# Performance work log

Measured on AMD Instinct MI355X. Metric: run time of the kernel, lower is better.

The kernel has to match this reference:

```python
import jax, jax.numpy as jnp
import numpy as np

# ---- config (mirrors cfg / init kwargs) ----
FEAT_STRIDE = 16
IM_DIMS = (1024, 1024)          # (height, width)
ANCHOR_SCALES = (8, 16, 32)
ANCHOR_RATIOS = (0.5, 1.0, 2.0)
PRE_NMS_TOPN = 6000             # eval mode (cfg_key=1)
POST_NMS_TOPN = 300
NMS_THRESH = 0.7
MIN_SIZE = 16


def _generate_base_anchors(base_size=16, ratios=ANCHOR_RATIOS, scales=ANCHOR_SCALES):
    """py-faster-rcnn generate_anchors, in numpy (static)."""
    def mk(ws, hs, xc, yc):
        return np.stack([xc - 0.5 * (ws - 1), yc - 0.5 * (hs - 1),
                         xc + 0.5 * (ws - 1), yc + 0.5 * (hs - 1)], axis=1)
    base = np.array([0, 0, base_size - 1, base_size - 1], dtype=np.float64)
    w = base[2] - base[0] + 1; h = base[3] - base[1] + 1
    xc = base[0] + 0.5 * (w - 1); yc = base[1] + 0.5 * (h - 1)
    # ratio enum
    size = w * h
    ws = np.round(np.sqrt(size / np.array(ratios)))
    hs = np.round(ws * np.array(ratios))
    ratio_anchors = mk(ws, hs, xc, yc)
    # scale enum
    out = []
    for a in ratio_anchors:
        aw = a[2] - a[0] + 1; ah = a[3] - a[1] + 1
        axc = a[0] + 0.5 * (aw - 1); ayc = a[1] + 0.5 * (ah - 1)
        out.append(mk(aw * np.array(scales), ah * np.array(scales), axc, ayc))
    return np.concatenate(out, axis=0).astype(np.float32)  # [A,4]


def _all_anchors(H, W):
    base = _generate_base_anchors()                       # [A,4]
    sx = np.arange(W) * FEAT_STRIDE
    sy = np.arange(H) * FEAT_STRIDE
    sx, sy = np.meshgrid(sx, sy)
    shifts = np.stack([sx.ravel(), sy.ravel(), sx.ravel(), sy.ravel()], axis=1)  # [H*W,4]
    anchors = shifts[:, None, :].astype(np.float32) + base[None, :, :]
    return anchors.reshape(-1, 4)                         # [H*W*A, 4]


def setup_inputs() -> dict:
    key = jax.random.key(0)
    k1, k2 = jax.random.split(key)
    H, W, A = 64, 64, 9
    rpn_cls_score = jax.random.normal(k1, (1, H, W, 2 * A), dtype=jnp.float32)
    rpn_bbox_pred = jax.random.normal(k2, (1, H, W, 4 * A), dtype=jnp.float32)
    return {"rpn_cls_score": rpn_cls_score, "rpn_bbox_pred": rpn_bbox_pred}


def _proposals(rpn_cls_score, rpn_bbox_pred):
    _, H, W, C2 = rpn_cls_score.shape
    A = C2 // 2
    # rpn_softmax: per-anchor 2-way softmax, foreground prob
    scores = jax.nn.softmax(rpn_cls_score.reshape(H, W, A, 2), axis=-1)[..., 1].reshape(-1)  # [N]
    deltas = rpn_bbox_pred.reshape(-1, 4)                  # [N,4]
    anchors = jnp.asarray(_all_anchors(H, W))              # [N,4]
    # bbox_transform_inv
    aw = anchors[:, 2] - anchors[:, 0] + 1.0
    ah = anchors[:, 3] - anchors[:, 1] + 1.0
    axc = anchors[:, 0] + 0.5 * aw
    ayc = anchors[:, 1] + 0.5 * ah
    dx, dy, dw, dh = deltas[:, 0], deltas[:, 1], deltas[:, 2], deltas[:, 3]
    pxc = dx * aw + axc; pyc = dy * ah + ayc
    pw = jnp.exp(dw) * aw; ph = jnp.exp(dh) * ah
    x1 = pxc - 0.5 * pw; y1 = pyc - 0.5 * ph
    x2 = pxc + 0.5 * pw; y2 = pyc + 0.5 * ph
    # clip to image
    im_h, im_w = IM_DIMS
    x1 = jnp.clip(x1, 0.0, im_w - 1.0); x2 = jnp.clip(x2, 0.0, im_w - 1.0)
    y1 = jnp.clip(y1, 0.0, im_h - 1.0); y2 = jnp.clip(y2, 0.0, im_h - 1.0)
    boxes = jnp.stack([x1, y1, x2, y2], axis=1)            # [N,4]
    # filter too-small boxes by masking their score
    valid = ((x2 - x1 + 1.0) >= MIN_SIZE) & ((y2 - y1 + 1.0) >= MIN_SIZE)
    scores = jnp.where(valid, scores, -jnp.inf)
    return boxes, scores


def _nms_keep(boxes, K):
    """Greedy NMS keep-mask over score-descending boxes [K,4]."""
    x1, y1, x2, y2 = boxes[:, 0], boxes[:, 1], boxes[:, 2], boxes[:, 3]
    areas = (x2 - x1 + 1.0) * (y2 - y1 + 1.0)
    ix1 = jnp.maximum(x1[:, None], x1[None, :])
    iy1 = jnp.maximum(y1[:, None], y1[None, :])
    ix2 = jnp.minimum(x2[:, None], x2[None, :])
    iy2 = jnp.minimum(y2[:, None], y2[None, :])
    iw = jnp.maximum(ix2 - ix1 + 1.0, 0.0)
    ih = jnp.maximum(iy2 - iy1 + 1.0, 0.0)
    inter = iw * ih
    iou = inter / (areas[:, None] + areas[None, :] - inter)  # [K,K]
    idxs = jnp.arange(K)
    def body(i, keep):
        sup = keep[i] & (iou[i] > NMS_THRESH) & (idxs > i)
        return keep & ~sup
    return jax.lax.fori_loop(0, K, body, jnp.ones((K,), bool))


def reference(rpn_cls_score, rpn_bbox_pred):
    boxes, scores = _proposals(rpn_cls_score, rpn_bbox_pred)
    K = min(PRE_NMS_TOPN, scores.shape[0])
    top_scores, order = jax.lax.top_k(scores, K)           # score-descending
    top_boxes = boxes[order]                               # [K,4]
    keep = _nms_keep(top_boxes, K)
    sel_scores = jnp.where(keep, top_scores, -jnp.inf)
    _, idx = jax.lax.top_k(sel_scores, POST_NMS_TOPN)      # kept, in score order
    out_boxes = top_boxes[idx]                             # [post,4]
    blob = jnp.concatenate([jnp.zeros((POST_NMS_TOPN, 1), out_boxes.dtype), out_boxes], axis=1)
    return blob                                            # [post,5] (batch_idx, x1,y1,x2,y2)
```

## Files before the change

kernel.cpp:

```cpp
#include <hip/hip_runtime.h>
#include <stdint.h>

typedef unsigned long long u64;
typedef unsigned int u32;

#define N_ANCH 36864
#define WGRID 64
#define A_PER 9
#define KTOP 6000
#define NOUT 300
#define NBIN 8192
#define NCHK 94
#define INF_BIN 0

__constant__ float c_ax1[9] = {-84.f,-176.f,-360.f,-56.f,-120.f,-248.f,-36.f,-80.f,-168.f};
__constant__ float c_ay1[9] = {-40.f,-88.f,-184.f,-56.f,-120.f,-248.f,-80.f,-168.f,-344.f};
__constant__ float c_aw[9]  = {184.f,368.f,736.f,128.f,256.f,512.f,88.f,176.f,352.f};
__constant__ float c_ah[9]  = {96.f,192.f,384.f,128.f,256.f,512.f,176.f,352.f,704.f};

__device__ __forceinline__ u32 binof(u32 u) {
    if (u < 0x80000000u) return 0u;
    if (u < 0xBF000000u) return 1u + ((u - 0x80000000u) >> 22);
    return 256u + ((u - 0xBF000000u) >> 11);
}

__global__ __launch_bounds__(1024) void proposal_kernel(const float* __restrict__ cls,
                                                        const float* __restrict__ dlt,
                                                        u64* __restrict__ keys,
                                                        float4* __restrict__ boxes,
                                                        u32* __restrict__ hist) {
    __shared__ u32 lh[NBIN];
    const int t = threadIdx.x;
    for (int b = t; b < NBIN; b += 1024) lh[b] = 0;
    __syncthreads();

    int i = blockIdx.x * 1024 + t;
    int a  = i % A_PER;
    int hw = i / A_PER;
    int wx = hw % WGRID;
    int hy = hw / WGRID;

    float l0 = cls[hw * 18 + 2 * a];
    float l1 = cls[hw * 18 + 2 * a + 1];
    float m  = fmaxf(l0, l1);
    float e0 = expf(l0 - m), e1 = expf(l1 - m);
    float s  = e1 / (e0 + e1);

    const float* d = dlt + hw * 36 + 4 * a;
    float dx = d[0], dy = d[1], dw = d[2], dh = d[3];
    float aw = c_aw[a], ah = c_ah[a];
    float axc = (c_ax1[a] + 16.f * (float)wx) + 0.5f * aw;
    float ayc = (c_ay1[a] + 16.f * (float)hy) + 0.5f * ah;

    float pxc = dx * aw + axc;
    float pyc = dy * ah + ayc;
    float pw  = expf(dw) * aw;
    float ph  = expf(dh) * ah;
    float x1 = pxc - 0.5f * pw, y1 = pyc - 0.5f * ph;
    float x2 = pxc + 0.5f * pw, y2 = pyc + 0.5f * ph;
    x1 = fminf(fmaxf(x1, 0.f), 1023.f);
    x2 = fminf(fmaxf(x2, 0.f), 1023.f);
    y1 = fminf(fmaxf(y1, 0.f), 1023.f);
    y2 = fminf(fmaxf(y2, 0.f), 1023.f);
    bool valid = ((x2 - x1 + 1.f) >= 16.f) && ((y2 - y1 + 1.f) >= 16.f);
    float sc = valid ? s : -__builtin_huge_valf();

    u32 sb  = __float_as_uint(sc);
    u32 ord = (sb & 0x80000000u) ? ~sb : (sb | 0x80000000u);
    u64 key = ((u64)ord << 32) | (u32)(~(u32)i);
    keys[i]  = key;
    boxes[i] = make_float4(x1, y1, x2, y2);

    u64 infb = __ballot(!valid);
    if (valid) {
        atomicAdd(&lh[binof(ord)], 1u);
    } else {
        int lane = t & 63;
        if (lane == __builtin_ctzll(infb))
            atomicAdd(&lh[INF_BIN], (u32)__popcll(infb));
    }
    __syncthreads();
    for (int b = t; b < NBIN; b += 1024) {
        u32 v = lh[b];
        if (v) atomicAdd(&hist[b], v);
    }
}

__global__ __launch_bounds__(1024) void scan_kernel(const u32* __restrict__ hist,
                                                    u32* __restrict__ binStart,
                                                    u32* __restrict__ gEV) {
    __shared__ u32 sh[1024];
    int t = threadIdx.x;
    if (t == 0) gEV[1] = KTOP;
    int hi = NBIN - 1 - 8 * t;
    u32 cnt[8];
    u32 sum = 0;
#pragma unroll
    for (int k = 0; k < 8; ++k) { cnt[k] = hist[hi - k]; sum += cnt[k]; }
    sh[t] = sum;
    __syncthreads();
    for (int d = 1; d < 1024; d <<= 1) {
        u32 v = (t >= d) ? sh[t - d] : 0;
        __syncthreads();
        sh[t] += v;
        __syncthreads();
    }
    u32 run = sh[t] - sum;
#pragma unroll
    for (int k = 0; k < 8; ++k) {
        int b = hi - k;
        binStart[b] = run;
        u32 end = run + cnt[k];
        if (run < KTOP && end >= KTOP) gEV[0] = end;
        run = end;
    }
}

__global__ void scatter_kernel(const u64* __restrict__ keys,
                               const u32* __restrict__ binStart,
                               u32* __restrict__ cursor,
                               u64* __restrict__ scat) {
    int i = blockIdx.x * blockDim.x + threadIdx.x;
    if (i >= N_ANCH) return;
    u64 k = keys[i];
    u32 b = binof((u32)(k >> 32));
    u32 s = binStart[b];
    if (s < KTOP) {
        u32 p = s + atomicAdd(&cursor[b], 1u);
        scat[p] = k;
    }
}

__global__ void rank_kernel(const u64* __restrict__ scat,
                            const u32* __restrict__ binStart,
                            const u32* __restrict__ hist,
                            const float4* __restrict__ boxes,
                            const u32* __restrict__ gEV,
                            float4* __restrict__ topBoxes,
                            int* __restrict__ gV) {
    int i = blockIdx.x * blockDim.x + threadIdx.x;
    u32 E = gEV[0];
    if (i >= (int)E) return;
    u64 k = scat[i];
    u32 b = binof((u32)(k >> 32));
    u32 s = binStart[b], c = hist[b];
    u32 r = s;
    for (u32 j = s; j < s + c; ++j) r += (scat[j] > k) ? 1u : 0u;
    if (r < KTOP) {
        int idx = (int)(~(u32)k);
        topBoxes[r] = boxes[idx];
        if (!(k >> 63)) atomicMin(gV, (int)r);
    }
}

__device__ __forceinline__ bool iou_gt(float4 a, float areaA, float4 b, float areaB) {
    float ix1 = fmaxf(a.x, b.x), iy1 = fmaxf(a.y, b.y);
    float ix2 = fminf(a.z, b.z), iy2 = fminf(a.w, b.w);
    float iw = fmaxf(ix2 - ix1 + 1.0f, 0.0f);
    float ih = fmaxf(iy2 - iy1 + 1.0f, 0.0f);
    float inter = iw * ih;
    float iou = inter / (areaA + areaB - inter);
    return iou > 0.7f;
}

__global__ __launch_bounds__(1024) void nms_out_kernel(const float4* __restrict__ topBoxes,
                                                       const u32* __restrict__ gEV,
                                                       float* __restrict__ out) {
    __shared__ float4 cbox[2][64];
    __shared__ float  ca[2][64];
    __shared__ u64    intra[2][64];
    __shared__ u64    supw[16];
    __shared__ u64    keepw[NCHK];
    __shared__ float4 kbox[NOUT];
    __shared__ float  karea[NOUT];
    __shared__ u32    scanbuf[1024];
    __shared__ int    s_nkept;

    const int t = threadIdx.x;
    const int lane = t & 63;
    const int w = t >> 6;
    if (t < NCHK) keepw[t] = 0;
    if (t == 0) s_nkept = 0;
    const int V = (int)gEV[1];
    const int nchunks = (V + 63) >> 6;

    if (t < 64) {
        float4 b = make_float4(0.f, 0.f, 0.f, 0.f);
        if (t < V) b = topBoxes[t];
        cbox[0][t] = b;
        ca[0][t]   = (b.z - b.x + 1.f) * (b.w - b.y + 1.f);
        intra[0][t] = 0;
    }
    __syncthreads();

    for (int c = 0; c < nchunks; ++c) {
        const int p = c & 1;
        const int base = c * 64;
        const int csz = min(64, V - base);
        const int nk = s_nkept;
        bool sup = false;
        if (lane < csz) {
            float4 bb = cbox[p][lane]; float ab = ca[p][lane];
            for (int k = w; k < nk; k += 16) {
                if (iou_gt(bb, ab, kbox[k], karea[k])) { sup = true; break; }
            }
        }
        u64 bal = __ballot(sup);
        if (lane == 0) supw[w] = bal;
        if (lane < csz) {
            float4 bb = cbox[p][lane]; float ab = ca[p][lane];
            u64 m = 0;
            int j0 = lane + 1;
            j0 += ((w - j0) % 16 + 16) % 16;
            for (int j = j0; j < csz; j += 16)
                if (iou_gt(bb, ab, cbox[p][j], ca[p][j])) m |= (1ULL << j);
            if (m) atomicOr(&intra[p][lane], m);
        }
        __syncthreads();
        if (w == 0) {
            u64 row = intra[p][lane];
            u64 sup64 = 0;
#pragma unroll
            for (int q = 0; q < 16; ++q) sup64 |= supw[q];
            u64 alive = ~sup64;
            if (csz < 64) alive &= ((1ULL << csz) - 1ULL);
            u64 cand = alive, kb = 0;
            const int nk_base = s_nkept;
            int nk2 = nk_base;
            while (cand && nk2 < NOUT) {
                int b = __builtin_ctzll(cand);
                cand &= cand - 1;
                kb |= (1ULL << b);
                ++nk2;
                cand &= ~__shfl(row, b, 64);
            }
            if ((kb >> lane) & 1ULL) {
                int pos = nk_base + __popcll(kb & ((1ULL << lane) - 1ULL));
                kbox[pos]  = cbox[p][lane];
                karea[pos] = ca[p][lane];
            }
            if (lane == 0) { keepw[c] = kb; s_nkept = nk2; }
        } else if (w == 1) {
            int nb = base + 64 + lane;
            float4 b = make_float4(0.f, 0.f, 0.f, 0.f);
            if (nb < V) b = topBoxes[nb];
            cbox[p ^ 1][lane] = b;
            ca[p ^ 1][lane]   = (b.z - b.x + 1.f) * (b.w - b.y + 1.f);
            intra[p ^ 1][lane] = 0;
        }
        __syncthreads();
        if (s_nkept >= NOUT) break;
    }

    const int n1 = s_nkept;
    for (int r = t; r < n1; r += 1024) {
        float4 b = kbox[r];
        out[r * 5 + 0] = 0.f;
        out[r * 5 + 1] = b.x; out[r * 5 + 2] = b.y;
        out[r * 5 + 3] = b.z; out[r * 5 + 4] = b.w;
    }
    if (n1 < NOUT) {
        __syncthreads();
        const int per = 6;
        int r0 = t * per, r1 = min(r0 + per, KTOP);
        u32 cnt = 0;
        for (int r = r0; r < r1; ++r)
            cnt += ((keepw[r >> 6] >> (r & 63)) & 1ULL) ? 0u : 1u;
        scanbuf[t] = cnt;
        __syncthreads();
        for (int d = 1; d < 1024; d <<= 1) {
            u32 v = (t >= d) ? scanbuf[t - d] : 0;
            __syncthreads();
            scanbuf[t] += v;
            __syncthreads();
        }
        int ord = n1 + (int)(scanbuf[t] - cnt);
        for (int r = r0; r < r1 && ord < NOUT; ++r) {
            if (!((keepw[r >> 6] >> (r & 63)) & 1ULL)) {
                float4 b = topBoxes[r];
                out[ord * 5 + 0] = 0.f;
                out[ord * 5 + 1] = b.x; out[ord * 5 + 2] = b.y;
                out[ord * 5 + 3] = b.z; out[ord * 5 + 4] = b.w;
                ++ord;
            }
        }
    }
}

extern "C" void kernel_launch(void* const* d_in, const int* in_sizes, int n_in,
                              void* d_out, int out_size, void* d_ws, size_t ws_size,
                              hipStream_t stream) {
    const float* cls = (const float*)d_in[0];
    const float* dlt = (const float*)d_in[1];
    float* out = (float*)d_out;
    char* ws = (char*)d_ws;
    u64*    keys     = (u64*)   (ws);
    u64*    scat     = (u64*)   (ws + 294912);
    float4* boxes    = (float4*)(ws + 589824);
    float4* topBoxes = (float4*)(ws + 1179648);
    u32*    hist     = (u32*)   (ws + 1275648);
    u32*    cursor   = (u32*)   (ws + 1308416);
    u32*    binStart = (u32*)   (ws + 1341184);
    u32*    gEV      = (u32*)   (ws + 1373952);

    hipMemsetAsync(hist, 0, 2 * NBIN * sizeof(u32), stream);
    proposal_kernel<<<36, 1024, 0, stream>>>(cls, dlt, keys, boxes, hist);
    scan_kernel<<<1, 1024, 0, stream>>>(hist, binStart, gEV);
    scatter_kernel<<<(N_ANCH + 255) / 256, 256, 0, stream>>>(keys, binStart, cursor, scat);
    rank_kernel<<<(N_ANCH + 255) / 256, 256, 0, stream>>>(scat, binStart, hist, boxes, gEV,
                                                          topBoxes, (int*)&gEV[1]);
    nms_out_kernel<<<1, 1024, 0, stream>>>(topBoxes, gEV, out);
}
```

Before: 118.2 us.

## Fuse proposal pipeline into one cooperative kernel and add spatial-grid NMS prefilter

Replaces the memset plus five separate launches with a single cooperative kernel of 36 blocks that uses grid.sync between the histogram, scan, scatter, rank and NMS phases. Keys stay in registers instead of round-tripping through global memory. It also adds a 64-bit coarse spatial occupancy signature per box, so IoU is only evaluated for pairs whose 128-pixel grid cells overlap. The costs are grid-wide barrier latency and cooperative-launch overhead, and the NMS tail still runs on only one block.

```diff
diff --git a/kernel.cpp b/kernel.cpp
--- a/kernel.cpp
+++ b/kernel.cpp
@@ -1,10 +1,14 @@
 #include <hip/hip_runtime.h>
+#include <hip/hip_cooperative_groups.h>
 #include <stdint.h>
+
+namespace cg = cooperative_groups;
 
 typedef unsigned long long u64;
 typedef unsigned int u32;
 
 #define N_ANCH 36864
+#define NBLK 36
 #define WGRID 64
 #define A_PER 9
 #define KTOP 6000
@@ -24,133 +28,12 @@
     return 256u + ((u - 0xBF000000u) >> 11);
 }
 
-__global__ __launch_bounds__(1024) void proposal_kernel(const float* __restrict__ cls,
-                                                        const float* __restrict__ dlt,
-                                                        u64* __restrict__ keys,
-                                                        float4* __restrict__ boxes,
-                                                        u32* __restrict__ hist) {
-    __shared__ u32 lh[NBIN];
-    const int t = threadIdx.x;
-    for (int b = t; b < NBIN; b += 1024) lh[b] = 0;
-    __syncthreads();
-
-    int i = blockIdx.x * 1024 + t;
-    int a  = i % A_PER;
-    int hw = i / A_PER;
-    int wx = hw % WGRID;
-    int hy = hw / WGRID;
-
-    float l0 = cls[hw * 18 + 2 * a];
-    float l1 = cls[hw * 18 + 2 * a + 1];
-    float m  = fmaxf(l0, l1);
-    float e0 = expf(l0 - m), e1 = expf(l1 - m);
-    float s  = e1 / (e0 + e1);
-
-    const float* d = dlt + hw * 36 + 4 * a;
-    float dx = d[0], dy = d[1], dw = d[2], dh = d[3];
-    float aw = c_aw[a], ah = c_ah[a];
-    float axc = (c_ax1[a] + 16.f * (float)wx) + 0.5f * aw;
-    float ayc = (c_ay1[a] + 16.f * (float)hy) + 0.5f * ah;
-
-    float pxc = dx * aw + axc;
-    float pyc = dy * ah + ayc;
-    float pw  = expf(dw) * aw;
-    float ph  = expf(dh) * ah;
-    float x1 = pxc - 0.5f * pw, y1 = pyc - 0.5f * ph;
-    float x2 = pxc + 0.5f * pw, y2 = pyc + 0.5f * ph;
-    x1 = fminf(fmaxf(x1, 0.f), 1023.f);
-    x2 = fminf(fmaxf(x2, 0.f), 1023.f);
-    y1 = fminf(fmaxf(y1, 0.f), 1023.f);
-    y2 = fminf(fmaxf(y2, 0.f), 1023.f);
-    bool valid = ((x2 - x1 + 1.f) >= 16.f) && ((y2 - y1 + 1.f) >= 16.f);
-    float sc = valid ? s : -__builtin_huge_valf();
-
-    u32 sb  = __float_as_uint(sc);
-    u32 ord = (sb & 0x80000000u) ? ~sb : (sb | 0x80000000u);
-    u64 key = ((u64)ord << 32) | (u32)(~(u32)i);
-    keys[i]  = key;
-    boxes[i] = make_float4(x1, y1, x2, y2);
-
-    u64 infb = __ballot(!valid);
-    if (valid) {
-        atomicAdd(&lh[binof(ord)], 1u);
-    } else {
-        int lane = t & 63;
-        if (lane == __builtin_ctzll(infb))
-            atomicAdd(&lh[INF_BIN], (u32)__popcll(infb));
-    }
-    __syncthreads();
-    for (int b = t; b < NBIN; b += 1024) {
-        u32 v = lh[b];
-        if (v) atomicAdd(&hist[b], v);
-    }
-}
-
-__global__ __launch_bounds__(1024) void scan_kernel(const u32* __restrict__ hist,
-                                                    u32* __restrict__ binStart,
-                                                    u32* __restrict__ gEV) {
-    __shared__ u32 sh[1024];
-    int t = threadIdx.x;
-    if (t == 0) gEV[1] = KTOP;
-    int hi = NBIN - 1 - 8 * t;
-    u32 cnt[8];
-    u32 sum = 0;
-#pragma unroll
-    for (int k = 0; k < 8; ++k) { cnt[k] = hist[hi - k]; sum += cnt[k]; }
-    sh[t] = sum;
-    __syncthreads();
-    for (int d = 1; d < 1024; d <<= 1) {
-        u32 v = (t >= d) ? sh[t - d] : 0;
-        __syncthreads();
-        sh[t] += v;
-        __syncthreads();
-    }
-    u32 run = sh[t] - sum;
-#pragma unroll
-    for (int k = 0; k < 8; ++k) {
-        int b = hi - k;
-        binStart[b] = run;
-        u32 end = run + cnt[k];
-        if (run < KTOP && end >= KTOP) gEV[0] = end;
-        run = end;
-    }
-}
-
-__global__ void scatter_kernel(const u64* __restrict__ keys,
-                               const u32* __restrict__ binStart,
-                               u32* __restrict__ cursor,
-                               u64* __restrict__ scat) {
-    int i = blockIdx.x * blockDim.x + threadIdx.x;
-    if (i >= N_ANCH) return;
-    u64 k = keys[i];
-    u32 b = binof((u32)(k >> 32));
-    u32 s = binStart[b];
-    if (s < KTOP) {
-        u32 p = s + atomicAdd(&cursor[b], 1u);
-        scat[p] = k;
-    }
-}
-
-__global__ void rank_kernel(const u64* __restrict__ scat,
-                            const u32* __restrict__ binStart,
-                            const u32* __restrict__ hist,
-                            const float4* __restrict__ boxes,
-                            const u32* __restrict__ gEV,
-                            float4* __restrict__ topBoxes,
-                            int* __restrict__ gV) {
-    int i = blockIdx.x * blockDim.x + threadIdx.x;
-    u32 E = gEV[0];
-    if (i >= (int)E) return;
-    u64 k = scat[i];
-    u32 b = binof((u32)(k >> 32));
-    u32 s = binStart[b], c = hist[b];
-    u32 r = s;
-    for (u32 j = s; j < s + c; ++j) r += (scat[j] > k) ? 1u : 0u;
-    if (r < KTOP) {
-        int idx = (int)(~(u32)k);
-        topBoxes[r] = boxes[idx];
-        if (!(k >> 63)) atomicMin(gV, (int)r);
-    }
+__device__ __forceinline__ u64 sigof(float4 b) {
+    int cx0 = (int)b.x >> 7, cx1 = (int)b.z >> 7;
+    int cy0 = (int)b.y >> 7, cy1 = (int)b.w >> 7;
+    u32 colm = (2u << cx1) - (1u << cx0);
+    u64 rowsel = ((~0ULL) >> (8 * (7 - cy1))) & ((~0ULL) << (8 * cy0));
+    return rowsel & (0x0101010101010101ULL * (u64)colm);
 }
 
 __device__ __forceinline__ bool iou_gt(float4 a, float areaA, float4 b, float areaB) {
@@ -163,20 +46,147 @@
     return iou > 0.7f;
 }
 
-__global__ __launch_bounds__(1024) void nms_out_kernel(const float4* __restrict__ topBoxes,
-                                                       const u32* __restrict__ gEV,
-                                                       float* __restrict__ out) {
+__global__ __launch_bounds__(1024) void fused_kernel(
+    const float* __restrict__ cls, const float* __restrict__ dlt,
+    u64* __restrict__ scat, float4* __restrict__ boxes,
+    float4* __restrict__ topBoxes, u32* __restrict__ hist,
+    u32* __restrict__ cursor, u32* __restrict__ binStart,
+    u32* __restrict__ gEV, float* __restrict__ out)
+{
+    cg::grid_group grid = cg::this_grid();
+    const int t = threadIdx.x;
+    const int gid = (int)blockIdx.x * 1024 + t;
+
+    __shared__ u32 lh[NBIN];
+    __shared__ u32 sh[1024];
+
+    if (gid < 2 * NBIN) hist[gid] = 0;
+    if (gid == 0) gEV[1] = KTOP;
+    for (int b = t; b < NBIN; b += 1024) lh[b] = 0;
+    __syncthreads();
+
+    const int i = gid;
+    {
+        int a  = i % A_PER;
+        int hw = i / A_PER;
+        int wx = hw % WGRID;
+        int hy = hw / WGRID;
+        float l0 = cls[hw * 18 + 2 * a];
+        float l1 = cls[hw * 18 + 2 * a + 1];
+        float m  = fmaxf(l0, l1);
+        float e0 = expf(l0 - m), e1 = expf(l1 - m);
+        float s  = e1 / (e0 + e1);
+
+        const float* d = dlt + hw * 36 + 4 * a;
+        float dx = d[0], dy = d[1], dw = d[2], dh = d[3];
+        float aw = c_aw[a], ah = c_ah[a];
+        float axc = (c_ax1[a] + 16.f * (float)wx) + 0.5f * aw;
+        float ayc = (c_ay1[a] + 16.f * (float)hy) + 0.5f * ah;
+        float pxc = dx * aw + axc;
+        float pyc = dy * ah + ayc;
+        float pw  = expf(dw) * aw;
+        float ph  = expf(dh) * ah;
+        float x1 = pxc - 0.5f * pw, y1 = pyc - 0.5f * ph;
+        float x2 = pxc + 0.5f * pw, y2 = pyc + 0.5f * ph;
+        x1 = fminf(fmaxf(x1, 0.f), 1023.f);
+        x2 = fminf(fmaxf(x2, 0.f), 1023.f);
+        y1 = fminf(fmaxf(y1, 0.f), 1023.f);
+        y2 = fminf(fmaxf(y2, 0.f), 1023.f);
+        bool valid = ((x2 - x1 + 1.f) >= 16.f) && ((y2 - y1 + 1.f) >= 16.f);
+        float sc = valid ? s : -__builtin_huge_valf();
+
+        u32 sb  = __float_as_uint(sc);
+        u32 ord = (sb & 0x80000000u) ? ~sb : (sb | 0x80000000u);
+        u64 key = ((u64)ord << 32) | (u32)(~(u32)i);
+        boxes[i] = make_float4(x1, y1, x2, y2);
+
+        u64 infb = __ballot(!valid);
+        if (valid) {
+            atomicAdd(&lh[binof(ord)], 1u);
+        } else if ((t & 63) == __builtin_ctzll(infb)) {
+            atomicAdd(&lh[INF_BIN], (u32)__popcll(infb));
+        }
+        __syncthreads();
+        __threadfence();
+        grid.sync();
+
+        for (int b = t; b < NBIN; b += 1024) {
+            u32 v = lh[b];
+            if (v) atomicAdd(&hist[b], v);
+        }
+        __threadfence();
+        grid.sync();
+
+        if (blockIdx.x == 0) {
+            int hi = NBIN - 1 - 8 * t;
+            u32 cnt[8];
+            u32 sum = 0;
+#pragma unroll
+            for (int k = 0; k < 8; ++k) { cnt[k] = hist[hi - k]; sum += cnt[k]; }
+            sh[t] = sum;
+            __syncthreads();
+            for (int dd = 1; dd < 1024; dd <<= 1) {
+                u32 v = (t >= dd) ? sh[t - dd] : 0;
+                __syncthreads();
+                sh[t] += v;
+                __syncthreads();
+            }
+            u32 run = sh[t] - sum;
+#pragma unroll
+            for (int k = 0; k < 8; ++k) {
+                int b = hi - k;
+                binStart[b] = run;
+                u32 end = run + cnt[k];
+                if (run < KTOP && end >= KTOP) gEV[0] = end;
+                run = end;
+            }
+        }
+        __threadfence();
+        grid.sync();
+
+        {
+            u32 b = binof(ord);
+            u32 s0 = binStart[b];
+            if (s0 < KTOP) {
+                u32 p = s0 + atomicAdd(&cursor[b], 1u);
+                scat[p] = key;
+            }
+        }
+        __threadfence();
+        grid.sync();
+    }
+
+    {
+        u32 E = gEV[0];
+        if (gid < (int)E) {
+            u64 k = scat[gid];
+            u32 b = binof((u32)(k >> 32));
+            u32 s0 = binStart[b], c = hist[b];
+            u32 r = s0;
+            for (u32 j = s0; j < s0 + c; ++j) r += (scat[j] > k) ? 1u : 0u;
+            if (r < KTOP) {
+                int idx = (int)(~(u32)k);
+                topBoxes[r] = boxes[idx];
+                if (!(k >> 63)) atomicMin((int*)&gEV[1], (int)r);
+            }
+        }
+    }
+    __threadfence();
+    grid.sync();
+
+    if (blockIdx.x != 0) return;
+
     __shared__ float4 cbox[2][64];
     __shared__ float  ca[2][64];
+    __shared__ u64    csig[2][64];
     __shared__ u64    intra[2][64];
     __shared__ u64    supw[16];
     __shared__ u64    keepw[NCHK];
     __shared__ float4 kbox[NOUT];
     __shared__ float  karea[NOUT];
-    __shared__ u32    scanbuf[1024];
+    __shared__ u64    ksig[NOUT];
     __shared__ int    s_nkept;
 
-    const int t = threadIdx.x;
     const int lane = t & 63;
     const int w = t >> 6;
     if (t < NCHK) keepw[t] = 0;
@@ -189,6 +199,7 @@
         if (t < V) b = topBoxes[t];
         cbox[0][t] = b;
         ca[0][t]   = (b.z - b.x + 1.f) * (b.w - b.y + 1.f);
+        csig[0][t] = sigof(b);
         intra[0][t] = 0;
     }
     __syncthreads();
@@ -200,20 +211,23 @@
         const int nk = s_nkept;
         bool sup = false;
         if (lane < csz) {
-            float4 bb = cbox[p][lane]; float ab = ca[p][lane];
+            float4 bb = cbox[p][lane]; float ab = ca[p][lane]; u64 sg = csig[p][lane];
             for (int k = w; k < nk; k += 16) {
-                if (iou_gt(bb, ab, kbox[k], karea[k])) { sup = true; break; }
+                if (sg & ksig[k]) {
+                    if (iou_gt(bb, ab, kbox[k], karea[k])) { sup = true; break; }
+                }
             }
         }
         u64 bal = __ballot(sup);
         if (lane == 0) supw[w] = bal;
         if (lane < csz) {
-            float4 bb = cbox[p][lane]; float ab = ca[p][lane];
+            float4 bb = cbox[p][lane]; float ab = ca[p][lane]; u64 sg = csig[p][lane];
             u64 m = 0;
             int j0 = lane + 1;
             j0 += ((w - j0) % 16 + 16) % 16;
             for (int j = j0; j < csz; j += 16)
-                if (iou_gt(bb, ab, cbox[p][j], ca[p][j])) m |= (1ULL << j);
+                if ((sg & csig[p][j]) && iou_gt(bb, ab, cbox[p][j], ca[p][j]))
+                    m |= (1ULL << j);
             if (m) atomicOr(&intra[p][lane], m);
         }
         __syncthreads();
@@ -238,6 +252,7 @@
                 int pos = nk_base + __popcll(kb & ((1ULL << lane) - 1ULL));
                 kbox[pos]  = cbox[p][lane];
                 karea[pos] = ca[p][lane];
+                ksig[pos]  = csig[p][lane];
             }
             if (lane == 0) { keepw[c] = kb; s_nkept = nk2; }
         } else if (w == 1) {
@@ -246,6 +261,7 @@
             if (nb < V) b = topBoxes[nb];
             cbox[p ^ 1][lane] = b;
             ca[p ^ 1][lane]   = (b.z - b.x + 1.f) * (b.w - b.y + 1.f);
+            csig[p ^ 1][lane] = sigof(b);
             intra[p ^ 1][lane] = 0;
         }
         __syncthreads();
@@ -266,22 +282,22 @@
         u32 cnt = 0;
         for (int r = r0; r < r1; ++r)
             cnt += ((keepw[r >> 6] >> (r & 63)) & 1ULL) ? 0u : 1u;
-        scanbuf[t] = cnt;
-        __syncthreads();
-        for (int d = 1; d < 1024; d <<= 1) {
-            u32 v = (t >= d) ? scanbuf[t - d] : 0;
+        sh[t] = cnt;
+        __syncthreads();
+        for (int dd = 1; dd < 1024; dd <<= 1) {
+            u32 v = (t >= dd) ? sh[t - dd] : 0;
             __syncthreads();
-            scanbuf[t] += v;
+            sh[t] += v;
             __syncthreads();
         }
-        int ord = n1 + (int)(scanbuf[t] - cnt);
-        for (int r = r0; r < r1 && ord < NOUT; ++r) {
+        int ord2 = n1 + (int)(sh[t] - cnt);
+        for (int r = r0; r < r1 && ord2 < NOUT; ++r) {
             if (!((keepw[r >> 6] >> (r & 63)) & 1ULL)) {
                 float4 b = topBoxes[r];
-                out[ord * 5 + 0] = 0.f;
-                out[ord * 5 + 1] = b.x; out[ord * 5 + 2] = b.y;
-                out[ord * 5 + 3] = b.z; out[ord * 5 + 4] = b.w;
-                ++ord;
+                out[ord2 * 5 + 0] = 0.f;
+                out[ord2 * 5 + 1] = b.x; out[ord2 * 5 + 2] = b.y;
+                out[ord2 * 5 + 3] = b.z; out[ord2 * 5 + 4] = b.w;
+                ++ord2;
             }
         }
     }
@@ -294,20 +310,17 @@
     const float* dlt = (const float*)d_in[1];
     float* out = (float*)d_out;
     char* ws = (char*)d_ws;
-    u64*    keys     = (u64*)   (ws);
-    u64*    scat     = (u64*)   (ws + 294912);
-    float4* boxes    = (float4*)(ws + 589824);
-    float4* topBoxes = (float4*)(ws + 1179648);
-    u32*    hist     = (u32*)   (ws + 1275648);
-    u32*    cursor   = (u32*)   (ws + 1308416);
-    u32*    binStart = (u32*)   (ws + 1341184);
-    u32*    gEV      = (u32*)   (ws + 1373952);
-
-    hipMemsetAsync(hist, 0, 2 * NBIN * sizeof(u32), stream);
-    proposal_kernel<<<36, 1024, 0, stream>>>(cls, dlt, keys, boxes, hist);
-    scan_kernel<<<1, 1024, 0, stream>>>(hist, binStart, gEV);
-    scatter_kernel<<<(N_ANCH + 255) / 256, 256, 0, stream>>>(keys, binStart, cursor, scat);
-    rank_kernel<<<(N_ANCH + 255) / 256, 256, 0, stream>>>(scat, binStart, hist, boxes, gEV,
-                                                          topBoxes, (int*)&gEV[1]);
-    nms_out_kernel<<<1, 1024, 0, stream>>>(topBoxes, gEV, out);
-}
+    u64*    scat     = (u64*)   (ws);
+    float4* boxes    = (float4*)(ws + 294912);
+    float4* topBoxes = (float4*)(ws + 884736);
+    u32*    hist     = (u32*)   (ws + 980736);
+    u32*    cursor   = (u32*)   (ws + 1013504);
+    u32*    binStart = (u32*)   (ws + 1046272);
+    u32*    gEV      = (u32*)   (ws + 1079040);
+
+    void* args[] = { (void*)&cls, (void*)&dlt, (void*)&scat, (void*)&boxes,
+                     (void*)&topBoxes, (void*)&hist, (void*)&cursor,
+                     (void*)&binStart, (void*)&gEV, (void*)&out };
+    hipLaunchCooperativeKernel((const void*)fused_kernel, dim3(NBLK), dim3(1024),
+                               args, 0, stream);
+}
```

Measured after the change: 210.2 us. +77.9%, slower.
